# Optimization experiments

Measured on AMD Instinct MI355X. Metric: run time of the kernel, lower is better.

Reference implementation:

```python
import jax, jax.numpy as jnp
import numpy as np

NEG_SLOPE = 0.2
EPS = 1e-16  # PyG softmax eps


def _gat_conv(x, src, dst, W, att_src, att_dst, bias, heads, out_ch):
    """PyG GATConv (eval mode, self-loops already appended, concat output)."""
    N = x.shape[0]
    xw = (x @ W).reshape(N, heads, out_ch)            # [N,H,C]
    a_src = jnp.sum(xw * att_src, axis=-1)            # [N,H]
    a_dst = jnp.sum(xw * att_dst, axis=-1)            # [N,H]
    e = jax.nn.leaky_relu(a_src[src] + a_dst[dst], NEG_SLOPE)  # [E,H]
    m = jax.ops.segment_max(e, dst, num_segments=N)   # [N,H] (self-loops -> no empty segs)
    e = jnp.exp(e - m[dst])
    denom = jax.ops.segment_sum(e, dst, num_segments=N)
    alpha = e / (denom[dst] + EPS)                    # [E,H]
    msg = xw[src] * alpha[:, :, None]                 # [E,H,C]
    out = jax.ops.segment_sum(msg, dst, num_segments=N)  # [N,H,C]
    return out.reshape(N, heads * out_ch) + bias


def setup_inputs() -> dict:
    key = jax.random.key(0)
    ks = jax.random.split(key, 12)
    N, E, F_in, H, C, NC = 20000, 320000, 512, 8, 64, 32
    x = jax.random.normal(ks[0], (N, F_in), dtype=jnp.float32)
    edge_index = jax.random.randint(ks[1], (2, E), 0, N, dtype=jnp.int64)
    g = lambda k, shape, fan: jax.random.normal(k, shape, dtype=jnp.float32) * (1.0 / np.sqrt(fan))
    return {
        "x": x,
        "edge_index": edge_index,
        "W1": g(ks[2], (F_in, H * C), F_in),
        "att_src1": g(ks[3], (H, C), C),
        "att_dst1": g(ks[4], (H, C), C),
        "b1": jnp.zeros((H * C,), dtype=jnp.float32),
        "W2": g(ks[5], (H * C, NC), H * C),
        "att_src2": g(ks[6], (1, NC), NC),
        "att_dst2": g(ks[7], (1, NC), NC),
        "b2": jnp.zeros((NC,), dtype=jnp.float32),
    }


def reference(x, edge_index, W1, att_src1, att_dst1, b1, W2, att_src2, att_dst2, b2):
    N = x.shape[0]
    H, C = att_src1.shape
    NC = att_src2.shape[1]
    # GATConv adds self-loops by default
    loops = jnp.arange(N, dtype=edge_index.dtype)
    src = jnp.concatenate([edge_index[0], loops])
    dst = jnp.concatenate([edge_index[1], loops])
    h = _gat_conv(x, src, dst, W1, att_src1, att_dst1, b1, H, C)
    h = jax.nn.elu(h)
    h = _gat_conv(h, src, dst, W2, att_src2, att_dst2, b2, 1, NC)
    return jax.nn.log_softmax(h, axis=1)
```

## Files before the change

kernel.cpp:

```cpp
#include <hip/hip_runtime.h>
#include <math.h>

#define NEG_SLOPE 0.2f
#define SM_EPS 1e-16f

typedef short short8 __attribute__((ext_vector_type(8)));
typedef float floatx4 __attribute__((ext_vector_type(4)));


__device__ inline unsigned short f2bf(float x) {
    unsigned int u = __float_as_uint(x);
    unsigned int r = (u + 0x7FFFu + ((u >> 16) & 1u)) >> 16;
    return (unsigned short)r;
}

__device__ inline float bf2f(unsigned short h) {
    return __uint_as_float(((unsigned int)h) << 16);
}

__device__ inline float bflo(unsigned int u) { return __uint_as_float(u << 16); }
__device__ inline float bfhi(unsigned int u) { return __uint_as_float(u & 0xFFFF0000u); }

__device__ __forceinline__ void gl_lds16(const unsigned short* g, unsigned short* l) {
    __builtin_amdgcn_global_load_lds(
        (const __attribute__((address_space(1))) unsigned int*)(g),
        (__attribute__((address_space(3))) unsigned int*)(l), 16, 0, 0);
}

__device__ inline void get_edge(const int* __restrict__ srcA, const int* __restrict__ dstA,
                                int e, int E, int& s, int& d) {
    if (e < E) { s = srcA[e]; d = dstA[e]; }
    else { s = e - E; d = e - E; }
}


__global__ __launch_bounds__(256) void k_prep(const float* __restrict__ x,
                                              unsigned short* __restrict__ xb,
                                              const float* __restrict__ W1,
                                              unsigned short* __restrict__ w1t,
                                              const float* __restrict__ W2,
                                              unsigned short* __restrict__ w2bt,
                                              const int* __restrict__ dstA,
                                              int E, int Ep,
                                              int* __restrict__ deg,
                                              int nblk_deg, int nblk_x) {
    __shared__ float tile[32][33];
    int bx = blockIdx.x;
    int t = threadIdx.x;
    if (bx < nblk_deg) {
        int e = bx * 256 + t;
        if (e < Ep) {
            int d = (e < E) ? dstA[e] : (e - E);
            atomicAdd(&deg[d], 1);
        }
    } else if (bx < nblk_deg + nblk_x) {
        int i = ((bx - nblk_deg) * 256 + t) * 4;
        float4 v = *(const float4*)(x + i);
        ushort4 o;
        o.x = f2bf(v.x); o.y = f2bf(v.y); o.z = f2bf(v.z); o.w = f2bf(v.w);
        *(ushort4*)(xb + i) = o;
    } else if (bx < nblk_deg + nblk_x + 256) {
        int b = bx - nblk_deg - nblk_x;
        int kb = (b & 15) * 32;
        int nb = (b >> 4) * 32;
        int tx = t & 31, ty = t >> 5;
        #pragma unroll
        for (int i = 0; i < 32; i += 8)
            tile[ty + i][tx] = W1[(size_t)(kb + ty + i) * 512 + nb + tx];
        __syncthreads();
        #pragma unroll
        for (int i = 0; i < 32; i += 8)
            w1t[(size_t)(nb + ty + i) * 512 + kb + tx] = f2bf(tile[tx][ty + i]);
    } else {
        int i = (bx - nblk_deg - nblk_x - 256) * 256 + t;
        int c = i >> 9, k = i & 511;
        w2bt[i] = f2bf(W2[k * 32 + c]);
    }
}


__global__ __launch_bounds__(256) void k_scan1(const int* __restrict__ deg, int* __restrict__ incl,
                                               int* __restrict__ part, int N) {
    __shared__ int sm[256];
    int t = threadIdx.x;
    int i = blockIdx.x * 256 + t;
    int v = (i < N) ? deg[i] : 0;
    sm[t] = v; __syncthreads();
    for (int o = 1; o < 256; o <<= 1) {
        int x = (t >= o) ? sm[t - o] : 0;
        __syncthreads();
        sm[t] += x;
        __syncthreads();
    }
    if (i < N) incl[i] = sm[t];
    if (t == 255) part[blockIdx.x] = sm[255];
}

__global__ __launch_bounds__(256) void k_scan3(const int* __restrict__ incl, const int* __restrict__ part,
                                               const int* __restrict__ deg, int* __restrict__ off,
                                               int* __restrict__ cursor, int N) {
    __shared__ int sm[256];
    int bx = blockIdx.x, t = threadIdx.x;
    int partial = 0;
    for (int i = t; i < bx; i += 256) partial += part[i];
    sm[t] = partial; __syncthreads();
    for (int o = 128; o > 0; o >>= 1) {
        if (t < o) sm[t] += sm[t + o];
        __syncthreads();
    }
    int base = sm[0];
    int i = bx * 256 + t;
    if (i >= N) return;
    int v = incl[i] + base;
    off[i + 1] = v;
    cursor[i] = v - deg[i];
    if (i == 0) off[0] = 0;
}

__global__ __launch_bounds__(256) void k_scatter(const int* __restrict__ srcA, const int* __restrict__ dstA,
                                                 int E, int Ep, int* __restrict__ cursor,
                                                 int* __restrict__ src_s) {
    int e = blockIdx.x * 256 + threadIdx.x;
    if (e >= Ep) return;
    int s, d; get_edge(srcA, dstA, e, E, s, d);
    int p = atomicAdd(&cursor[d], 1);
    src_s[p] = s;
}


__global__ __launch_bounds__(256) void k_gemm1_mfma(const unsigned short* __restrict__ A,
                                                    const unsigned short* __restrict__ Bt,
                                                    const float* __restrict__ att_s,
                                                    const float* __restrict__ att_d,
                                                    unsigned short* __restrict__ C,
                                                    float* __restrict__ a_sd,
                                                    float* __restrict__ a_dd, int M) {
    const int K = 512;
    __shared__ unsigned short As[2][128 * 64];
    __shared__ unsigned short Bs[2][128 * 64];
    int t = threadIdx.x;
    int lane = t & 63;
    int w = t >> 6;
    int row0 = blockIdx.x * 128;
    int col0 = blockIdx.y * 128;
    int wm = (w >> 1) * 64, wn = (w & 1) * 64;
    int l15 = lane & 15, q = lane >> 4;

    int srow = w * 32 + (lane >> 3);
    int sgc = ((lane & 7) ^ (lane >> 3)) * 8;

    floatx4 acc[4][4] = {};

    auto STAGE = [&](int buf, int k0) {
        #pragma unroll
        for (int i = 0; i < 4; ++i) {
            int r = srow + i * 8;
            gl_lds16(A  + (size_t)(row0 + r) * K + k0 + sgc, &As[buf][(w * 32 + i * 8) * 64]);
            gl_lds16(Bt + (size_t)(col0 + r) * K + k0 + sgc, &Bs[buf][(w * 32 + i * 8) * 64]);
        }
    };

    STAGE(0, 0);
    asm volatile("s_waitcnt vmcnt(0)" ::: "memory");
    __builtin_amdgcn_s_barrier();

    int buf = 0;
    for (int k0 = 0; k0 < K; k0 += 64) {
        if (k0 + 64 < K) {
            STAGE(buf ^ 1, k0 + 64);
            asm volatile("s_waitcnt vmcnt(8)" ::: "memory");
        } else {
            asm volatile("s_waitcnt vmcnt(0)" ::: "memory");
        }
        __builtin_amdgcn_s_barrier();
        __builtin_amdgcn_sched_barrier(0);
        #pragma unroll
        for (int ks = 0; ks < 2; ++ks) {
            short8 af[4], bfr[4];
            int sw = ((ks * 4 + q) ^ (l15 & 7)) * 8;
            #pragma unroll
            for (int i = 0; i < 4; ++i)
                af[i] = *(const short8*)(&As[buf][(wm + i * 16 + l15) * 64 + sw]);
            #pragma unroll
            for (int j = 0; j < 4; ++j)
                bfr[j] = *(const short8*)(&Bs[buf][(wn + j * 16 + l15) * 64 + sw]);
            #pragma unroll
            for (int i = 0; i < 4; ++i)
                #pragma unroll
                for (int j = 0; j < 4; ++j)
                    acc[i][j] = __builtin_amdgcn_mfma_f32_16x16x32_bf16(af[i], bfr[j], acc[i][j], 0, 0, 0);
        }
        asm volatile("s_waitcnt lgkmcnt(0)" ::: "memory");
        __builtin_amdgcn_sched_barrier(0);
        __builtin_amdgcn_s_barrier();
        buf ^= 1;
    }

    #pragma unroll
    for (int i = 0; i < 4; ++i) {
        #pragma unroll
        for (int p = 0; p < 4; ++p) {
            int r = row0 + wm + i * 16 + q * 4 + p;
            if (r < M) {
                #pragma unroll
                for (int j = 0; j < 4; ++j) {
                    int c = col0 + wn + j * 16 + l15;
                    C[(size_t)r * 512 + c] = f2bf(acc[i][j][p]);
                }
            }
        }
    }

    int hh = blockIdx.y * 2 + (w & 1);
    float asr[4], adr[4];
    #pragma unroll
    for (int j = 0; j < 4; ++j) {
        asr[j] = att_s[hh * 64 + j * 16 + l15];
        adr[j] = att_d[hh * 64 + j * 16 + l15];
    }
    #pragma unroll
    for (int i = 0; i < 4; ++i) {
        #pragma unroll
        for (int p = 0; p < 4; ++p) {
            float ds = 0.f, dd = 0.f;
            #pragma unroll
            for (int j = 0; j < 4; ++j) {
                ds = fmaf(acc[i][j][p], asr[j], ds);
                dd = fmaf(acc[i][j][p], adr[j], dd);
            }
            #pragma unroll
            for (int mk = 1; mk <= 8; mk <<= 1) {
                ds += __shfl_xor(ds, mk);
                dd += __shfl_xor(dd, mk);
            }
            int r = row0 + wm + i * 16 + q * 4 + p;
            if (l15 == 0 && r < M) {
                a_sd[(size_t)hh * M + r] = ds;
                a_dd[(size_t)hh * M + r] = dd;
            }
        }
    }
}


__global__ __launch_bounds__(256) void k_l1(const unsigned short* __restrict__ xw,
                                            const float* __restrict__ a_s,
                                            const float* __restrict__ a_d,
                                            const int* __restrict__ off,
                                            const int* __restrict__ src_s,
                                            const float* __restrict__ bias,
                                            unsigned short* __restrict__ hout, int N) {
    int wid = threadIdx.x >> 6, lane = threadIdx.x & 63;
    int h = blockIdx.x & 7;
    int n = (blockIdx.x >> 3) * 32 + wid * 8 + (lane >> 3);
    int li = lane & 7;
    if (n >= N) return;
    int p0 = off[n], p1 = off[n + 1];
    const float* ash = a_s + (size_t)h * N;
    float adv = a_d[(size_t)h * N + n];
    const size_t cbase = (size_t)h * 64 + (size_t)li * 8;

    float acc[8] = {};
    float s = 0.f;
    int p = p0;
    if (p + 4 <= p1) {
        int s0 = src_s[p], s1 = src_s[p + 1], s2 = src_s[p + 2], s3 = src_s[p + 3];
        while (true) {
            const uint4 u0 = *(const uint4*)(xw + (size_t)s0 * 512 + cbase);
            const uint4 u1 = *(const uint4*)(xw + (size_t)s1 * 512 + cbase);
            const uint4 u2 = *(const uint4*)(xw + (size_t)s2 * 512 + cbase);
            const uint4 u3 = *(const uint4*)(xw + (size_t)s3 * 512 + cbase);
            float e0 = ash[s0] + adv; e0 = e0 > 0.f ? e0 : NEG_SLOPE * e0;
            float e1 = ash[s1] + adv; e1 = e1 > 0.f ? e1 : NEG_SLOPE * e1;
            float e2 = ash[s2] + adv; e2 = e2 > 0.f ? e2 : NEG_SLOPE * e2;
            float e3 = ash[s3] + adv; e3 = e3 > 0.f ? e3 : NEG_SLOPE * e3;
            int np = p + 4;
            bool more = (np + 4 <= p1);
            int t0 = 0, t1 = 0, t2 = 0, t3 = 0;
            if (more) {
                t0 = src_s[np]; t1 = src_s[np + 1];
                t2 = src_s[np + 2]; t3 = src_s[np + 3];
            }
            float w0 = __expf(e0);
            float w1 = __expf(e1);
            float w2 = __expf(e2);
            float w3 = __expf(e3);
            s += (w0 + w1) + (w2 + w3);
            acc[0] = fmaf(w0, bflo(u0.x), acc[0]); acc[1] = fmaf(w0, bfhi(u0.x), acc[1]);
            acc[2] = fmaf(w0, bflo(u0.y), acc[2]); acc[3] = fmaf(w0, bfhi(u0.y), acc[3]);
            acc[4] = fmaf(w0, bflo(u0.z), acc[4]); acc[5] = fmaf(w0, bfhi(u0.z), acc[5]);
            acc[6] = fmaf(w0, bflo(u0.w), acc[6]); acc[7] = fmaf(w0, bfhi(u0.w), acc[7]);
            acc[0] = fmaf(w1, bflo(u1.x), acc[0]); acc[1] = fmaf(w1, bfhi(u1.x), acc[1]);
            acc[2] = fmaf(w1, bflo(u1.y), acc[2]); acc[3] = fmaf(w1, bfhi(u1.y), acc[3]);
            acc[4] = fmaf(w1, bflo(u1.z), acc[4]); acc[5] = fmaf(w1, bfhi(u1.z), acc[5]);
            acc[6] = fmaf(w1, bflo(u1.w), acc[6]); acc[7] = fmaf(w1, bfhi(u1.w), acc[7]);
            acc[0] = fmaf(w2, bflo(u2.x), acc[0]); acc[1] = fmaf(w2, bfhi(u2.x), acc[1]);
            acc[2] = fmaf(w2, bflo(u2.y), acc[2]); acc[3] = fmaf(w2, bfhi(u2.y), acc[3]);
            acc[4] = fmaf(w2, bflo(u2.z), acc[4]); acc[5] = fmaf(w2, bfhi(u2.z), acc[5]);
            acc[6] = fmaf(w2, bflo(u2.w), acc[6]); acc[7] = fmaf(w2, bfhi(u2.w), acc[7]);
            acc[0] = fmaf(w3, bflo(u3.x), acc[0]); acc[1] = fmaf(w3, bfhi(u3.x), acc[1]);
            acc[2] = fmaf(w3, bflo(u3.y), acc[2]); acc[3] = fmaf(w3, bfhi(u3.y), acc[3]);
            acc[4] = fmaf(w3, bflo(u3.z), acc[4]); acc[5] = fmaf(w3, bfhi(u3.z), acc[5]);
            acc[6] = fmaf(w3, bflo(u3.w), acc[6]); acc[7] = fmaf(w3, bfhi(u3.w), acc[7]);
            p = np;
            if (!more) break;
            s0 = t0; s1 = t1; s2 = t2; s3 = t3;
        }
    }
    for (; p < p1; ++p) {
        int s0 = src_s[p];
        const uint4 u0 = *(const uint4*)(xw + (size_t)s0 * 512 + cbase);
        float e0 = ash[s0] + adv; e0 = e0 > 0.f ? e0 : NEG_SLOPE * e0;
        float w0 = __expf(e0);
        s += w0;
        acc[0] = fmaf(w0, bflo(u0.x), acc[0]); acc[1] = fmaf(w0, bfhi(u0.x), acc[1]);
        acc[2] = fmaf(w0, bflo(u0.y), acc[2]); acc[3] = fmaf(w0, bfhi(u0.y), acc[3]);
        acc[4] = fmaf(w0, bflo(u0.z), acc[4]); acc[5] = fmaf(w0, bfhi(u0.z), acc[5]);
        acc[6] = fmaf(w0, bflo(u0.w), acc[6]); acc[7] = fmaf(w0, bfhi(u0.w), acc[7]);
    }

    float inv = 1.f / (s + SM_EPS);
    unsigned int ov[4];
    #pragma unroll
    for (int j = 0; j < 4; ++j) {
        float v0 = acc[2 * j] * inv     + bias[cbase + 2 * j];
        float v1 = acc[2 * j + 1] * inv + bias[cbase + 2 * j + 1];
        v0 = v0 > 0.f ? v0 : __expf(v0) - 1.f;
        v1 = v1 > 0.f ? v1 : __expf(v1) - 1.f;
        ov[j] = (unsigned int)f2bf(v0) | ((unsigned int)f2bf(v1) << 16);
    }
    *(uint4*)(hout + (size_t)n * 512 + cbase) = make_uint4(ov[0], ov[1], ov[2], ov[3]);
}


__global__ __launch_bounds__(256) void k_gemm2_mfma(const unsigned short* __restrict__ A,
                                                    const unsigned short* __restrict__ Bt,
                                                    const float* __restrict__ att_s,
                                                    const float* __restrict__ att_d,
                                                    unsigned short* __restrict__ O,
                                                    float* __restrict__ a_s, float* __restrict__ a_d,
                                                    int M) {
    const int K = 512;
    __shared__ unsigned short As[64 * 512];
    __shared__ unsigned short Bs[32 * 512];
    int t = threadIdx.x;
    int lane = t & 63;
    int w = t >> 6;
    int row0 = blockIdx.x * 64;
    int l15 = lane & 15, q = lane >> 4;

    #pragma unroll
    for (int i = 0; i < 16; ++i) {
        int r = w * 16 + i;
        gl_lds16(A + (size_t)(row0 + r) * K + ((lane ^ (r & 7)) << 3), &As[r * 512]);
    }
    #pragma unroll
    for (int i = 0; i < 8; ++i) {
        int r = w * 8 + i;
        gl_lds16(Bt + (size_t)r * K + ((lane ^ (r & 7)) << 3), &Bs[r * 512]);
    }
    __syncthreads();

    floatx4 acc[2] = {};
    int ra = w * 16 + l15;
    int rb0 = l15, rb1 = 16 + l15;
    #pragma unroll
    for (int k0 = 0; k0 < K; k0 += 32) {
        int cc = (k0 >> 3) + q;
        short8 af = *(const short8*)(&As[ra * 512 + ((cc ^ (ra & 7)) << 3)]);
        short8 b0 = *(const short8*)(&Bs[rb0 * 512 + ((cc ^ (rb0 & 7)) << 3)]);
        short8 b1 = *(const short8*)(&Bs[rb1 * 512 + ((cc ^ (rb1 & 7)) << 3)]);
        acc[0] = __builtin_amdgcn_mfma_f32_16x16x32_bf16(af, b0, acc[0], 0, 0, 0);
        acc[1] = __builtin_amdgcn_mfma_f32_16x16x32_bf16(af, b1, acc[1], 0, 0, 0);
    }

    float as_lo = att_s[l15], as_hi = att_s[16 + l15];
    float ad_lo = att_d[l15], ad_hi = att_d[16 + l15];
    #pragma unroll
    for (int p = 0; p < 4; ++p) {
        int r = row0 + w * 16 + q * 4 + p;
        bool ok = r < M;
        float v0 = acc[0][p], v1 = acc[1][p];
        if (ok) {
            O[(size_t)r * 32 + l15]      = f2bf(v0);
            O[(size_t)r * 32 + 16 + l15] = f2bf(v1);
        }
        float ds = v0 * as_lo + v1 * as_hi;
        float dd = v0 * ad_lo + v1 * ad_hi;
        #pragma unroll
        for (int mk = 1; mk <= 8; mk <<= 1) {
            ds += __shfl_xor(ds, mk);
            dd += __shfl_xor(dd, mk);
        }
        if (ok && l15 == 0) { a_s[r] = ds; a_d[r] = dd; }
    }
}


__global__ __launch_bounds__(256) void k_l2(const unsigned short* __restrict__ hw2,
                                            const float* __restrict__ a_s,
                                            const float* __restrict__ a_d,
                                            const int* __restrict__ off,
                                            const int* __restrict__ src_s,
                                            const float* __restrict__ bias,
                                            float* __restrict__ outp, int N) {
    int wid = threadIdx.x >> 6, lane = threadIdx.x & 63;
    int n = blockIdx.x * 4 + wid;
    if (n >= N) return;
    int p0 = off[n], p1 = off[n + 1];
    float adv = a_d[n];
    int e8 = lane >> 3;
    int li = lane & 7;
    const int cbase = li * 4;

    float acc[4] = {};
    float s = 0.f;
    int p = p0;
    for (; p + 16 <= p1; p += 16) {
        int sA = src_s[p + e8];
        int sB = src_s[p + 8 + e8];
        const uint2 uA = *(const uint2*)(hw2 + (size_t)sA * 32 + cbase);
        const uint2 uB = *(const uint2*)(hw2 + (size_t)sB * 32 + cbase);
        float eA = a_s[sA] + adv; eA = eA > 0.f ? eA : NEG_SLOPE * eA;
        float eB = a_s[sB] + adv; eB = eB > 0.f ? eB : NEG_SLOPE * eB;
        float wA = __expf(eA);
        float wB = __expf(eB);
        s += wA + wB;
        acc[0] = fmaf(wA, bflo(uA.x), acc[0]); acc[1] = fmaf(wA, bfhi(uA.x), acc[1]);
        acc[2] = fmaf(wA, bflo(uA.y), acc[2]); acc[3] = fmaf(wA, bfhi(uA.y), acc[3]);
        acc[0] = fmaf(wB, bflo(uB.x), acc[0]); acc[1] = fmaf(wB, bfhi(uB.x), acc[1]);
        acc[2] = fmaf(wB, bflo(uB.y), acc[2]); acc[3] = fmaf(wB, bfhi(uB.y), acc[3]);
    }
    for (; p + 8 <= p1; p += 8) {
        int sA = src_s[p + e8];
        const uint2 uA = *(const uint2*)(hw2 + (size_t)sA * 32 + cbase);
        float eA = a_s[sA] + adv; eA = eA > 0.f ? eA : NEG_SLOPE * eA;
        float wA = __expf(eA);
        s += wA;
        acc[0] = fmaf(wA, bflo(uA.x), acc[0]); acc[1] = fmaf(wA, bfhi(uA.x), acc[1]);
        acc[2] = fmaf(wA, bflo(uA.y), acc[2]); acc[3] = fmaf(wA, bfhi(uA.y), acc[3]);
    }
    if (p < p1) {
        int nb = p1 - p;
        bool val = e8 < nb;
        int sA = src_s[val ? p + e8 : p];
        const uint2 uA = *(const uint2*)(hw2 + (size_t)sA * 32 + cbase);
        float eA = a_s[sA] + adv; eA = eA > 0.f ? eA : NEG_SLOPE * eA;
        float wA = val ? __expf(eA) : 0.f;
        s += wA;
        acc[0] = fmaf(wA, bflo(uA.x), acc[0]); acc[1] = fmaf(wA, bfhi(uA.x), acc[1]);
        acc[2] = fmaf(wA, bflo(uA.y), acc[2]); acc[3] = fmaf(wA, bfhi(uA.y), acc[3]);
    }

    #pragma unroll
    for (int mk = 8; mk <= 32; mk <<= 1) {
        s += __shfl_xor(s, mk);
        #pragma unroll
        for (int j = 0; j < 4; ++j) acc[j] += __shfl_xor(acc[j], mk);
    }

    float inv = 1.f / (s + SM_EPS);
    float v[4];
    #pragma unroll
    for (int j = 0; j < 4; ++j) v[j] = acc[j] * inv + bias[cbase + j];

    float mx = fmaxf(fmaxf(v[0], v[1]), fmaxf(v[2], v[3]));
    mx = fmaxf(mx, __shfl_xor(mx, 1));
    mx = fmaxf(mx, __shfl_xor(mx, 2));
    mx = fmaxf(mx, __shfl_xor(mx, 4));
    float sum = 0.f;
    #pragma unroll
    for (int j = 0; j < 4; ++j) sum += __expf(v[j] - mx);
    sum += __shfl_xor(sum, 1);
    sum += __shfl_xor(sum, 2);
    sum += __shfl_xor(sum, 4);
    float lse = __logf(sum);
    if (e8 == 0) {
        float4 o = make_float4(v[0] - mx - lse, v[1] - mx - lse,
                               v[2] - mx - lse, v[3] - mx - lse);
        *(float4*)(outp + (size_t)n * 32 + cbase) = o;
    }
}


extern "C" void kernel_launch(void* const* d_in, const int* in_sizes, int n_in,
                              void* d_out, int out_size, void* d_ws, size_t ws_size,
                              hipStream_t stream) {
    const float* x   = (const float*)d_in[0];
    const int*   ei  = (const int*)d_in[1];
    const float* W1  = (const float*)d_in[2];
    const float* as1 = (const float*)d_in[3];
    const float* ad1 = (const float*)d_in[4];
    const float* b1  = (const float*)d_in[5];
    const float* W2  = (const float*)d_in[6];
    const float* as2 = (const float*)d_in[7];
    const float* ad2 = (const float*)d_in[8];
    const float* b2  = (const float*)d_in[9];
    float* out = (float*)d_out;

    const int F = 512;
    const int N = in_sizes[0] / F;
    const int E = in_sizes[1] / 2;
    const int Ep = E + N;
    const int* srcA = ei;
    const int* dstA = ei + E;

    char* w = (char*)d_ws;
    auto alloc = [&](size_t b) -> void* {
        void* p = (void*)w;
        w += (b + 255) & ~(size_t)255;
        return p;
    };
    unsigned short* xbf  = (unsigned short*)alloc((size_t)N * 512 * 2);
    unsigned short* w1t  = (unsigned short*)alloc((size_t)512 * 512 * 2);
    unsigned short* w2bt = (unsigned short*)alloc((size_t)32 * 512 * 2);
    unsigned short* xw1  = (unsigned short*)alloc((size_t)N * 512 * 2);
    unsigned short* hbuf = (unsigned short*)alloc((size_t)N * 512 * 2);
    float* a_s1 = (float*)alloc((size_t)N * 8 * 4);
    float* a_d1 = (float*)alloc((size_t)N * 8 * 4);
    unsigned short* hw2 = (unsigned short*)alloc((size_t)N * 32 * 2);
    float* a_s2 = (float*)alloc((size_t)N * 4);
    float* a_d2 = (float*)alloc((size_t)N * 4);
    int* deg    = (int*)alloc((size_t)N * 4);
    int* incl   = (int*)alloc((size_t)N * 4);
    int* part   = (int*)alloc(256 * 4);
    int* off    = (int*)alloc((size_t)(N + 1) * 4);
    int* cursor = (int*)alloc((size_t)N * 4);
    int* src_s  = (int*)alloc((size_t)Ep * 4);

    int egrid = (Ep + 255) / 256;
    int sgrid = (N + 255) / 256;
    int ngrid4 = (N + 3) / 4;
    int nblk_x = (N * 512 / 4) / 256;
    int nblk_w2 = (32 * 512 + 255) / 256;

    hipMemsetAsync(deg, 0, (size_t)N * 4, stream);

    k_prep<<<egrid + nblk_x + 256 + nblk_w2, 256, 0, stream>>>(
        x, xbf, W1, w1t, W2, w2bt, dstA, E, Ep, deg, egrid, nblk_x);

    k_scan1<<<sgrid, 256, 0, stream>>>(deg, incl, part, N);
    k_scan3<<<sgrid, 256, 0, stream>>>(incl, part, deg, off, cursor, N);
    k_scatter<<<egrid, 256, 0, stream>>>(srcA, dstA, E, Ep, cursor, src_s);

    {
        dim3 g1((N + 127) / 128, 512 / 128);
        k_gemm1_mfma<<<g1, 256, 0, stream>>>(xbf, w1t, as1, ad1, xw1, a_s1, a_d1, N);
    }
    {
        int ngrid32 = (N + 31) / 32;
        k_l1<<<ngrid32 * 8, 256, 0, stream>>>(xw1, a_s1, a_d1, off, src_s, b1, hbuf, N);
    }

    k_gemm2_mfma<<<(N + 63) / 64, 256, 0, stream>>>(hbuf, w2bt, as2, ad2, hw2, a_s2, a_d2, N);
    k_l2<<<ngrid4, 256, 0, stream>>>(hw2, a_s2, a_d2, off, src_s, b2, out, N);
}
```

Before: 223.2 us.

## Fuse scan kernels via grid-wide spin barrier and shrink GEMM1 tiles

The two prefix-scan kernels are merged into one. It publishes per-block partial sums and spins on an atomic counter until every block is done, which removes one launch and the intermediate incl buffer. The counter is zeroed by extending the existing deg memset, and correctness assumes all 79 blocks are co-resident. GEMM1 moves from 128x128 tiles with K-step 64 to 64x128 tiles with K-step 32, using a smaller LDS footprint, an occupancy hint of 4 blocks, and a new swizzle. This doubles the grid for better CU coverage at 20000 rows, at the cost of less operand reuse and more barriers per K.

```diff
diff --git a/kernel.cpp b/kernel.cpp
--- a/kernel.cpp
+++ b/kernel.cpp
@@ -79,11 +79,15 @@
 }
 
 
-__global__ __launch_bounds__(256) void k_scan1(const int* __restrict__ deg, int* __restrict__ incl,
-                                               int* __restrict__ part, int N) {
+__global__ __launch_bounds__(256) void k_scan_fused(const int* __restrict__ deg,
+                                                    int* __restrict__ part,
+                                                    int* __restrict__ done,
+                                                    int* __restrict__ off,
+                                                    int* __restrict__ cursor,
+                                                    int N, int nblk) {
     __shared__ int sm[256];
-    int t = threadIdx.x;
-    int i = blockIdx.x * 256 + t;
+    int bx = blockIdx.x, t = threadIdx.x;
+    int i = bx * 256 + t;
     int v = (i < N) ? deg[i] : 0;
     sm[t] = v; __syncthreads();
     for (int o = 1; o < 256; o <<= 1) {
@@ -92,29 +96,31 @@
         sm[t] += x;
         __syncthreads();
     }
-    if (i < N) incl[i] = sm[t];
-    if (t == 255) part[blockIdx.x] = sm[255];
-}
-
-__global__ __launch_bounds__(256) void k_scan3(const int* __restrict__ incl, const int* __restrict__ part,
-                                               const int* __restrict__ deg, int* __restrict__ off,
-                                               int* __restrict__ cursor, int N) {
-    __shared__ int sm[256];
-    int bx = blockIdx.x, t = threadIdx.x;
+    int incl_v = sm[t];
+    if (t == 255) {
+        part[bx] = sm[255];
+        __threadfence();
+        atomicAdd(done, 1);
+    }
+    if (t == 0) {
+        while (atomicAdd(done, 0) < nblk) { }
+        __threadfence();
+    }
+    __syncthreads();
     int partial = 0;
-    for (int i = t; i < bx; i += 256) partial += part[i];
+    for (int j = t; j < bx; j += 256) partial += atomicAdd(&part[j], 0);
     sm[t] = partial; __syncthreads();
     for (int o = 128; o > 0; o >>= 1) {
         if (t < o) sm[t] += sm[t + o];
         __syncthreads();
     }
     int base = sm[0];
-    int i = bx * 256 + t;
-    if (i >= N) return;
-    int v = incl[i] + base;
-    off[i + 1] = v;
-    cursor[i] = v - deg[i];
-    if (i == 0) off[0] = 0;
+    if (i < N) {
+        int vv = incl_v + base;
+        off[i + 1] = vv;
+        cursor[i] = vv - v;
+        if (i == 0) off[0] = 0;
+    }
 }
 
 __global__ __launch_bounds__(256) void k_scatter(const int* __restrict__ srcA, const int* __restrict__ dstA,
@@ -128,68 +134,63 @@
 }
 
 
-__global__ __launch_bounds__(256) void k_gemm1_mfma(const unsigned short* __restrict__ A,
-                                                    const unsigned short* __restrict__ Bt,
-                                                    const float* __restrict__ att_s,
-                                                    const float* __restrict__ att_d,
-                                                    unsigned short* __restrict__ C,
-                                                    float* __restrict__ a_sd,
-                                                    float* __restrict__ a_dd, int M) {
+__global__ __launch_bounds__(256, 4) void k_gemm1_mfma(const unsigned short* __restrict__ A,
+                                                       const unsigned short* __restrict__ Bt,
+                                                       const float* __restrict__ att_s,
+                                                       const float* __restrict__ att_d,
+                                                       unsigned short* __restrict__ C,
+                                                       float* __restrict__ a_sd,
+                                                       float* __restrict__ a_dd, int M) {
     const int K = 512;
-    __shared__ unsigned short As[2][128 * 64];
-    __shared__ unsigned short Bs[2][128 * 64];
+    __shared__ unsigned short As[2][64 * 32];
+    __shared__ unsigned short Bs[2][128 * 32];
     int t = threadIdx.x;
     int lane = t & 63;
     int w = t >> 6;
-    int row0 = blockIdx.x * 128;
+    int row0 = blockIdx.x * 64;
     int col0 = blockIdx.y * 128;
-    int wm = (w >> 1) * 64, wn = (w & 1) * 64;
+    int wm = (w >> 1) * 32, wn = (w & 1) * 64;
     int l15 = lane & 15, q = lane >> 4;
 
-    int srow = w * 32 + (lane >> 3);
-    int sgc = ((lane & 7) ^ (lane >> 3)) * 8;
-
-    floatx4 acc[4][4] = {};
+    int srl = lane >> 2;
+    int sgc = ((lane & 3) ^ ((lane >> 3) & 3)) * 8;
+
+    floatx4 acc[2][4] = {};
 
     auto STAGE = [&](int buf, int k0) {
-        #pragma unroll
-        for (int i = 0; i < 4; ++i) {
-            int r = srow + i * 8;
-            gl_lds16(A  + (size_t)(row0 + r) * K + k0 + sgc, &As[buf][(w * 32 + i * 8) * 64]);
-            gl_lds16(Bt + (size_t)(col0 + r) * K + k0 + sgc, &Bs[buf][(w * 32 + i * 8) * 64]);
-        }
+        gl_lds16(A  + (size_t)(row0 + w * 16 + srl) * K + k0 + sgc, &As[buf][(w * 16) * 32]);
+        gl_lds16(Bt + (size_t)(col0 + w * 32 + srl) * K + k0 + sgc, &Bs[buf][(w * 32) * 32]);
+        gl_lds16(Bt + (size_t)(col0 + w * 32 + 16 + srl) * K + k0 + sgc, &Bs[buf][(w * 32 + 16) * 32]);
     };
 
     STAGE(0, 0);
     asm volatile("s_waitcnt vmcnt(0)" ::: "memory");
     __builtin_amdgcn_s_barrier();
 
+    int swz = (l15 >> 1) & 3;
     int buf = 0;
-    for (int k0 = 0; k0 < K; k0 += 64) {
-        if (k0 + 64 < K) {
-            STAGE(buf ^ 1, k0 + 64);
-            asm volatile("s_waitcnt vmcnt(8)" ::: "memory");
+    for (int k0 = 0; k0 < K; k0 += 32) {
+        if (k0 + 32 < K) {
+            STAGE(buf ^ 1, k0 + 32);
+            asm volatile("s_waitcnt vmcnt(3)" ::: "memory");
         } else {
             asm volatile("s_waitcnt vmcnt(0)" ::: "memory");
         }
         __builtin_amdgcn_s_barrier();
         __builtin_amdgcn_sched_barrier(0);
-        #pragma unroll
-        for (int ks = 0; ks < 2; ++ks) {
-            short8 af[4], bfr[4];
-            int sw = ((ks * 4 + q) ^ (l15 & 7)) * 8;
-            #pragma unroll
-            for (int i = 0; i < 4; ++i)
-                af[i] = *(const short8*)(&As[buf][(wm + i * 16 + l15) * 64 + sw]);
+        short8 af[2], bfr[4];
+        int sw = (q ^ swz) << 3;
+        #pragma unroll
+        for (int i = 0; i < 2; ++i)
+            af[i] = *(const short8*)(&As[buf][(wm + i * 16 + l15) * 32 + sw]);
+        #pragma unroll
+        for (int j = 0; j < 4; ++j)
+            bfr[j] = *(const short8*)(&Bs[buf][(wn + j * 16 + l15) * 32 + sw]);
+        #pragma unroll
+        for (int i = 0; i < 2; ++i)
             #pragma unroll
             for (int j = 0; j < 4; ++j)
-                bfr[j] = *(const short8*)(&Bs[buf][(wn + j * 16 + l15) * 64 + sw]);
-            #pragma unroll
-            for (int i = 0; i < 4; ++i)
-                #pragma unroll
-                for (int j = 0; j < 4; ++j)
-                    acc[i][j] = __builtin_amdgcn_mfma_f32_16x16x32_bf16(af[i], bfr[j], acc[i][j], 0, 0, 0);
-        }
+                acc[i][j] = __builtin_amdgcn_mfma_f32_16x16x32_bf16(af[i], bfr[j], acc[i][j], 0, 0, 0);
         asm volatile("s_waitcnt lgkmcnt(0)" ::: "memory");
         __builtin_amdgcn_sched_barrier(0);
         __builtin_amdgcn_s_barrier();
@@ -197,7 +198,7 @@
     }
 
     #pragma unroll
-    for (int i = 0; i < 4; ++i) {
+    for (int i = 0; i < 2; ++i) {
         #pragma unroll
         for (int p = 0; p < 4; ++p) {
             int r = row0 + wm + i * 16 + q * 4 + p;
@@ -219,7 +220,7 @@
         adr[j] = att_d[hh * 64 + j * 16 + l15];
     }
     #pragma unroll
-    for (int i = 0; i < 4; ++i) {
+    for (int i = 0; i < 2; ++i) {
         #pragma unroll
         for (int p = 0; p < 4; ++p) {
             float ds = 0.f, dd = 0.f;
@@ -522,11 +523,13 @@
     float* a_s2 = (float*)alloc((size_t)N * 4);
     float* a_d2 = (float*)alloc((size_t)N * 4);
     int* deg    = (int*)alloc((size_t)N * 4);
+    int* done   = (int*)alloc(256);
     int* incl   = (int*)alloc((size_t)N * 4);
     int* part   = (int*)alloc(256 * 4);
     int* off    = (int*)alloc((size_t)(N + 1) * 4);
     int* cursor = (int*)alloc((size_t)N * 4);
     int* src_s  = (int*)alloc((size_t)Ep * 4);
+    (void)incl;
 
     int egrid = (Ep + 255) / 256;
     int sgrid = (N + 255) / 256;
@@ -534,17 +537,16 @@
     int nblk_x = (N * 512 / 4) / 256;
     int nblk_w2 = (32 * 512 + 255) / 256;
 
-    hipMemsetAsync(deg, 0, (size_t)N * 4, stream);
+    hipMemsetAsync(deg, 0, (((size_t)N * 4 + 255) & ~(size_t)255) + 256, stream);
 
     k_prep<<<egrid + nblk_x + 256 + nblk_w2, 256, 0, stream>>>(
         x, xbf, W1, w1t, W2, w2bt, dstA, E, Ep, deg, egrid, nblk_x);
 
-    k_scan1<<<sgrid, 256, 0, stream>>>(deg, incl, part, N);
-    k_scan3<<<sgrid, 256, 0, stream>>>(incl, part, deg, off, cursor, N);
+    k_scan_fused<<<sgrid, 256, 0, stream>>>(deg, part, done, off, cursor, N, sgrid);
     k_scatter<<<egrid, 256, 0, stream>>>(srcA, dstA, E, Ep, cursor, src_s);
 
     {
-        dim3 g1((N + 127) / 128, 512 / 128);
+        dim3 g1((N + 63) / 64, 512 / 128);
         k_gemm1_mfma<<<g1, 256, 0, stream>>>(xbf, w1t, as1, ad1, xw1, a_s1, a_d1, N);
     }
     {
```

Result: no change. 224.1 us (+0.4%).
